# Kernel tuning notes

Hardware: AMD Instinct MI355X
Metric: run time of the kernel (lower is better)

Reference implementation:

```python
import jax, jax.numpy as jnp
import numpy as np

B, R, L, D, V, P = 128, 30, 60, 300, 50000, 3

def setup_inputs() -> dict:
    key = jax.random.key(0)
    ks = jax.random.split(key, 24)
    u = lambda k, shp: jax.random.uniform(k, shp, jnp.float32, -0.1, 0.1)
    inp = {
        'user_reviews': jax.random.randint(ks[0], (B, R, L), 0, V),
        'item_reviews': jax.random.randint(ks[1], (B, R, L), 0, V),
        'user_emb': u(ks[2], (V, D)),
        'item_emb': u(ks[3], (V, D)),
        'g1_w': u(ks[4], (D, D)), 'g1_b': u(ks[5], (D,)),
        'g2_w': u(ks[6], (D, D)), 'g2_b': u(ks[7], (D,)),
        # per-pointer review-level co-attention params (gumbel=True, pooling=max)
        'Mr': jax.random.normal(ks[8], (P, D, D)),
        'Wur': jax.random.normal(ks[9], (P, D, D)) * 0.05, 'bur': jnp.zeros((P, D)),
        'Wir': jax.random.normal(ks[10], (P, D, D)) * 0.05, 'bir': jnp.zeros((P, D)),
        # per-pointer word-level co-attention params (gumbel=False, pooling=avg)
        'Mw': jax.random.normal(ks[11], (P, D, D)),
        'Wuw': jax.random.normal(ks[12], (P, D, D)) * 0.05, 'buw': jnp.zeros((P, D)),
        'Wiw': jax.random.normal(ks[13], (P, D, D)) * 0.05, 'biw': jnp.zeros((P, D)),
        # FM params, pred_in_dim = 2*P*D (pointer_agg='concat')
        'fm_w0': jnp.zeros((1,)),
        'fm_w': jnp.zeros((2 * P * D,)),
        'fm_v': jax.random.normal(ks[14], (2 * P * D, 10)) * 0.01,
    }
    return inp

def _review_gate(embs, g1_w, g1_b, g2_w, g2_b):
    # embs: [B,R,L,D] -> [B,R,D]
    s = embs.sum(2)
    return jax.nn.sigmoid(s @ g1_w.T + g1_b) * jnp.tanh(s @ g2_w.T + g2_b)

def _coatt_scores(u_fea, i_fea, Wu, bu, Wi, bi, M):
    u = u_fea @ Wu.T + bu
    i = i_fea @ Wi.T + bi
    return jnp.einsum('brd,de,bse->brs', u, M, i)  # [B,R,R] or [B,L,L]

def reference(user_reviews, item_reviews, user_emb, item_emb,
              g1_w, g1_b, g2_w, g2_b,
              Mr, Wur, bur, Wir, bir,
              Mw, Wuw, buw, Wiw, biw,
              fm_w0, fm_w, fm_v):
    gkey = jax.random.key(42)
    u_embs = user_emb[user_reviews]  # [B,R,L,D]
    i_embs = item_emb[item_reviews]
    u_rev = _review_gate(u_embs, g1_w, g1_b, g2_w, g2_b)  # [B,R,D]
    i_rev = _review_gate(i_embs, g1_w, g1_b, g2_w, g2_b)
    u_reps, i_reps = [], []
    for p in range(P):
        # review-level co-attention, max pooling, gumbel hard (top-1 pointer)
        s = _coatt_scores(u_rev, i_rev, Wur[p], bur[p], Wir[p], bir[p], Mr[p])
        u_score = s.max(2)   # [B,R]
        i_score = s.max(1)   # [B,R]
        gu = jax.random.gumbel(jax.random.fold_in(gkey, 2 * p), u_score.shape)
        gi = jax.random.gumbel(jax.random.fold_in(gkey, 2 * p + 1), i_score.shape)
        # hard one-hot bmm gather + .long() re-embed == argmax review select
        # (the .long() cast in torch severs the straight-through grad path)
        idx_u = jnp.argmax(u_score + gu, axis=1)  # [B]
        idx_i = jnp.argmax(i_score + gi, axis=1)
        u_tok = jnp.take_along_axis(user_reviews, idx_u[:, None, None], axis=1)[:, 0]  # [B,L]
        i_tok = jnp.take_along_axis(item_reviews, idx_i[:, None, None], axis=1)[:, 0]
        u_words = user_emb[u_tok]  # [B,L,D]
        i_words = item_emb[i_tok]
        # word-level co-attention, avg pooling, soft attention
        s2 = _coatt_scores(u_words, i_words, Wuw[p], buw[p], Wiw[p], biw[p], Mw[p])
        p_u = jax.nn.softmax(s2.mean(2), axis=1)  # [B,L]
        p_i = jax.nn.softmax(s2.mean(1), axis=1)
        u_reps.append(jnp.einsum('bld,bl->bd', u_words, p_u))
        i_reps.append(jnp.einsum('bld,bl->bd', i_words, p_i))
    u_fea = jnp.concatenate(u_reps, axis=1)  # [B, P*D] (pointer_agg='concat')
    i_fea = jnp.concatenate(i_reps, axis=1)
    joint = jnp.concatenate([u_fea, i_fea], axis=1)  # [B, 2*P*D]; dropout is identity (eval)
    # Factorization Machine
    linear = fm_w0 + jnp.sum(fm_w * joint, axis=1, keepdims=True)
    inter = 0.5 * jnp.sum((joint @ fm_v) ** 2 - (joint ** 2) @ (fm_v ** 2), axis=1, keepdims=True)
    return (linear + inter)[:, 0]  # [B]
```

## Files before the change

### kernel.cpp

```cpp
#include <hip/hip_runtime.h>
#include <stdint.h>
#include <math.h>


__host__ __device__ static inline void tf2x32(uint32_t k0, uint32_t k1,
                                              uint32_t x0, uint32_t x1,
                                              uint32_t* o0, uint32_t* o1) {
  uint32_t ks[3] = {k0, k1, k0 ^ k1 ^ 0x1BD11BDAu};
  x0 += ks[0]; x1 += ks[1];
  const int rotA[4] = {13, 15, 26, 6};
  const int rotB[4] = {17, 29, 16, 24};
#pragma unroll
  for (int i = 0; i < 5; ++i) {
    const int* rot = ((i & 1) == 0) ? rotA : rotB;
#pragma unroll
    for (int j = 0; j < 4; ++j) {
      x0 += x1;
      x1 = (x1 << rot[j]) | (x1 >> (32 - rot[j]));
      x1 ^= x0;
    }
    x0 += ks[(i + 1) % 3];
    x1 += ks[(i + 2) % 3] + (uint32_t)(i + 1);
  }
  *o0 = x0; *o1 = x1;
}

struct GKeys { uint32_t v[12]; };
struct Ptr6 {
  const float* X[6];
  const float* W[6];
  const float* Bb[6];
  float*       Y[6];
};

__device__ static inline float jax_gumbel32(uint32_t k0, uint32_t k1, uint32_t idx) {
  uint32_t o0, o1;
  tf2x32(k0, k1, 0u, idx, &o0, &o1);
  uint32_t bits = o0 ^ o1;
  float f = __uint_as_float((bits >> 9) | 0x3f800000u) - 1.0f;
  float u = (f > 0.0f) ? f : 1.17549435e-38f;
  return -logf(-logf(u));
}

#define MODE_NN 0
#define MODE_NT 1
#define MODE_TN 2

template <int MODE, bool BIAS>
__device__ __forceinline__ void gemm_tile(float* __restrict__ sm,
                                          const float* __restrict__ X,
                                          const float* __restrict__ W,
                                          const float* __restrict__ bias,
                                          float* __restrict__ Y,
                                          float* __restrict__ Yt,
                                          int M, int bm, int n0, int t) {
  float (*Xs)[68] = (float(*)[68])sm;
  float (*Ws_)[68] = (float(*)[68])(sm + 20 * 68);
  const bool act = t < 256;
  int tm4 = ((t >> 4) & 15) * 4;
  int tn4 = (t & 15) * 4;
  float acc[4][4] = {{0.f}};
  int xm = t >> 2;
  int xk = (t & 3) * 5;
  for (int k0 = 0; k0 < 300; k0 += 20) {
    if (act) {
      if (MODE == MODE_TN) {
#pragma unroll
        for (int i = 0; i < 5; ++i) {
          int flat = t + i * 256;
          int kk = flat >> 6, nn = flat & 63;
          int r = bm + nn;
          Xs[kk][nn] = (r < 300) ? X[(size_t)(k0 + kk) * 300 + r] : 0.f;
        }
      } else {
        int rr = bm + xm; if (rr >= M) rr = M - 1;
        const float* xp = X + (size_t)rr * 300 + k0 + xk;
#pragma unroll
        for (int j = 0; j < 5; ++j) Xs[xk + j][xm] = xp[j];
      }
      if (MODE == MODE_NT) {
        int d = n0 + xm;
        bool ok = d < 300;
        const float* wp = W + (size_t)d * 300 + k0 + xk;
#pragma unroll
        for (int j = 0; j < 5; ++j) Ws_[xk + j][xm] = ok ? wp[j] : 0.f;
      } else {
#pragma unroll
        for (int i = 0; i < 5; ++i) {
          int flat = t + i * 256;
          int kk = flat >> 6, nn = flat & 63;
          int col = n0 + nn;
          Ws_[kk][nn] = (col < 300) ? W[(size_t)(k0 + kk) * 300 + col] : 0.f;
        }
      }
    }
    __syncthreads();
    if (act) {
#pragma unroll
      for (int kk = 0; kk < 20; ++kk) {
        const float4 a = *(const float4*)&Xs[kk][tm4];
        const float4 w = *(const float4*)&Ws_[kk][tn4];
        float av[4] = {a.x, a.y, a.z, a.w};
        float wv[4] = {w.x, w.y, w.z, w.w};
#pragma unroll
        for (int i = 0; i < 4; ++i)
#pragma unroll
          for (int j = 0; j < 4; ++j)
            acc[i][j] = fmaf(av[i], wv[j], acc[i][j]);
      }
    }
    __syncthreads();
  }
  if (!act) return;
  float bv[4] = {0.f, 0.f, 0.f, 0.f};
  if (BIAS) {
#pragma unroll
    for (int j = 0; j < 4; ++j) {
      int col = n0 + tn4 + j;
      if (col < 300) bv[j] = bias[col];
    }
  }
#pragma unroll
  for (int i = 0; i < 4; ++i) {
    int row = bm + tm4 + i;
    if (row < M) {
      float* yp = Y + (size_t)row * 300 + n0 + tn4;
#pragma unroll
      for (int j = 0; j < 4; ++j) {
        int col = n0 + tn4 + j;
        if (col < 300) yp[j] = acc[i][j] + bv[j];
      }
    }
  }
  if (Yt) {
#pragma unroll
    for (int i = 0; i < 4; ++i) {
      int row = bm + tm4 + i;
      if (row < 300) {
#pragma unroll
        for (int j = 0; j < 4; ++j) {
          int col = n0 + tn4 + j;
          if (col < 300) Yt[(size_t)col * 300 + row] = acc[i][j];
        }
      }
    }
  }
}

__global__ __launch_bounds__(256)
void weights_kernel(const float* __restrict__ Wur, const float* __restrict__ Mr,
                    const float* __restrict__ Mw, const float* __restrict__ Wiw,
                    const float* __restrict__ Wuw,
                    const float* __restrict__ bur, const float* __restrict__ buw,
                    const float* __restrict__ biw,
                    float* __restrict__ Wp, float* __restrict__ A1,
                    float* __restrict__ CGH, float* __restrict__ Bp) {
  __shared__ __align__(16) float arena[2720];
  int bid = blockIdx.x, t = threadIdx.x;
  if (bid < 75) {
    int z = bid / 25, r = bid % 25;
    gemm_tile<MODE_TN, false>(arena, Wur + (size_t)z * 90000, Mr + (size_t)z * 90000,
                              nullptr, Wp + (size_t)z * 90000, nullptr,
                              300, (r / 5) * 64, (r % 5) * 64, t);
  } else if (bid < 150) {
    int zi = bid - 75, z = zi / 25, r = zi % 25;
    gemm_tile<MODE_NN, false>(arena, Mw + (size_t)z * 90000, Wiw + (size_t)z * 90000,
                              nullptr, A1 + (size_t)z * 90000, nullptr,
                              300, (r / 5) * 64, (r % 5) * 64, t);
  } else {
    int z = bid - 150;
    float* vb = arena;
    float* t1s = arena + 304;
    float* t2s = arena + 608;
    const float* Mwz = Mw + (size_t)z * 90000;
    const float* Wuwz = Wuw + (size_t)z * 90000;
    const float* Wiwz = Wiw + (size_t)z * 90000;
    const float* Mrz = Mr + (size_t)z * 90000;
    for (int k = t; k < 300; k += 256) vb[k] = biw[z * 300 + k];
    __syncthreads();
    for (int e = t; e < 300; e += 256) {
      float a = 0.f;
      for (int k = 0; k < 300; ++k) a = fmaf(Mwz[(size_t)e * 300 + k], vb[k], a);
      t1s[e] = a;
    }
    __syncthreads();
    for (int k = t; k < 300; k += 256) {
      float a = 0.f;
      for (int d = 0; d < 300; ++d) a = fmaf(Wuwz[(size_t)d * 300 + k], t1s[d], a);
      CGH[(size_t)(2 * z) * 300 + k] = a;
    }
    __syncthreads();
    for (int d = t; d < 300; d += 256) vb[d] = buw[z * 300 + d];
    __syncthreads();
    for (int e = t; e < 300; e += 256) {
      float a = 0.f;
      for (int d = 0; d < 300; ++d) a = fmaf(Mwz[(size_t)d * 300 + e], vb[d], a);
      t2s[e] = a;
    }
    __syncthreads();
    for (int k = t; k < 300; k += 256) {
      float a = 0.f;
      for (int e = 0; e < 300; ++e) a = fmaf(Wiwz[(size_t)e * 300 + k], t2s[e], a);
      CGH[(size_t)(2 * z + 1) * 300 + k] = a;
    }
    __syncthreads();
    for (int d = t; d < 300; d += 256) vb[d] = bur[z * 300 + d];
    __syncthreads();
    for (int e = t; e < 300; e += 256) {
      float a = 0.f;
      for (int d = 0; d < 300; ++d) a = fmaf(Mrz[(size_t)d * 300 + e], vb[d], a);
      Bp[z * 300 + e] = a;
    }
  }
}

__global__ __launch_bounds__(320)
void gather_kernel(const int* __restrict__ uRevs, const int* __restrict__ iRevs,
                   const float* __restrict__ uEmb, const float* __restrict__ iEmb,
                   float* __restrict__ S) {
  int bid = blockIdx.x;
  int t = threadIdx.x;
  __shared__ int toks[4][60];
  if (t < 240) {
    int rr = t / 60, l = t - rr * 60;
    int grow = bid * 4 + rr;
    int side = grow / 3840;
    int row = grow - side * 3840;
    const int* revs = side ? iRevs : uRevs;
    toks[rr][l] = revs[row * 60 + l];
  }
  __syncthreads();
  if (t < 300) {
    int sub = t / 75;
    int q4 = (t - sub * 75) * 4;
    int grow = bid * 4 + sub;
    int side = grow / 3840;
    const float* emb = side ? iEmb : uEmb;
    const int* tk = toks[sub];
    float ax = 0.f, ay = 0.f, az = 0.f, aw = 0.f;
#pragma unroll
    for (int l0 = 0; l0 < 60; l0 += 10) {
      float4 v[10];
#pragma unroll
      for (int qq = 0; qq < 10; ++qq)
        v[qq] = *(const float4*)&emb[(size_t)tk[l0 + qq] * 300 + q4];
#pragma unroll
      for (int qq = 0; qq < 10; ++qq) {
        ax += v[qq].x; ay += v[qq].y; az += v[qq].z; aw += v[qq].w;
      }
    }
    float4 r = {ax, ay, az, aw};
    *(float4*)&S[(size_t)grow * 300 + q4] = r;
  }
}

__global__ __launch_bounds__(256)
void gate_kernel(const float* __restrict__ S,
                 const float* __restrict__ g1w, const float* __restrict__ g1b,
                 const float* __restrict__ g2w, const float* __restrict__ g2b,
                 float* __restrict__ REV,
                 const float* __restrict__ Wuw, const float* __restrict__ A1,
                 float* __restrict__ KG, float* __restrict__ KGT) {
  __shared__ __align__(16) float arena[4080];
  int bid = blockIdx.x, t = threadIdx.x;
  if (bid < 600) {
    float (*Xs)[68] = (float(*)[68])arena;
    float (*Ws1)[68] = (float(*)[68])(arena + 1360);
    float (*Ws2)[68] = (float(*)[68])(arena + 2720);
    int bm = (bid / 5) * 64;
    int n0 = (bid % 5) * 64;
    int tm4 = (t >> 4) * 4;
    int tn4 = (t & 15) * 4;
    float acc1[4][4] = {{0.f}};
    float acc2[4][4] = {{0.f}};
    int xm = t >> 2;
    int xk = (t & 3) * 5;
    for (int k0 = 0; k0 < 300; k0 += 20) {
      const float* xp = S + (size_t)(bm + xm) * 300 + k0 + xk;
#pragma unroll
      for (int j = 0; j < 5; ++j) Xs[xk + j][xm] = xp[j];
      {
        int dIdx = n0 + xm;
        bool ok = dIdx < 300;
        const float* wp1 = g1w + (size_t)dIdx * 300 + k0 + xk;
        const float* wp2 = g2w + (size_t)dIdx * 300 + k0 + xk;
#pragma unroll
        for (int j = 0; j < 5; ++j) Ws1[xk + j][xm] = ok ? wp1[j] : 0.f;
#pragma unroll
        for (int j = 0; j < 5; ++j) Ws2[xk + j][xm] = ok ? wp2[j] : 0.f;
      }
      __syncthreads();
#pragma unroll
      for (int kk = 0; kk < 20; ++kk) {
        const float4 a = *(const float4*)&Xs[kk][tm4];
        const float4 w1 = *(const float4*)&Ws1[kk][tn4];
        const float4 w2 = *(const float4*)&Ws2[kk][tn4];
        float av[4] = {a.x, a.y, a.z, a.w};
        float w1v[4] = {w1.x, w1.y, w1.z, w1.w};
        float w2v[4] = {w2.x, w2.y, w2.z, w2.w};
#pragma unroll
        for (int i = 0; i < 4; ++i)
#pragma unroll
          for (int j = 0; j < 4; ++j) {
            acc1[i][j] = fmaf(av[i], w1v[j], acc1[i][j]);
            acc2[i][j] = fmaf(av[i], w2v[j], acc2[i][j]);
          }
      }
      __syncthreads();
    }
#pragma unroll
    for (int i = 0; i < 4; ++i) {
      int row = bm + tm4 + i;
      float* yp = REV + (size_t)row * 300 + n0 + tn4;
#pragma unroll
      for (int j = 0; j < 4; ++j) {
        int col = n0 + tn4 + j;
        if (col < 300) {
          float a = acc1[i][j] + g1b[col];
          float b = acc2[i][j] + g2b[col];
          yp[j] = (1.f / (1.f + expf(-a))) * tanhf(b);
        }
      }
    }
  } else {
    int zi = bid - 600, z = zi / 25, r = zi % 25;
    gemm_tile<MODE_TN, false>(arena, Wuw + (size_t)z * 90000, A1 + (size_t)z * 90000,
                              nullptr, KG + (size_t)z * 90000,
                              KGT + (size_t)z * 90000,
                              300, (r / 5) * 64, (r % 5) * 64, t);
  }
}

__global__ __launch_bounds__(256)
void rev128_kernel(Ptr6 P) {
  int z = blockIdx.z;
  const bool nt = z >= 3;
  const float* __restrict__ X = P.X[z];
  const float* __restrict__ W = P.W[z];
  const float* __restrict__ bias = P.Bb[z];
  float* __restrict__ Y = P.Y[z];
  __shared__ __align__(16) float Xs[20][136];
  __shared__ __align__(16) float Ws_[20][68];
  int t = threadIdx.x;
  int bm = blockIdx.x * 128, n0 = blockIdx.y * 64;
  int tm8 = (t >> 4) * 8, tn4 = (t & 15) * 4;
  float acc[8][4] = {{0.f}};
  int xm = t >> 1, xk = (t & 1) * 10;
  int wm = t >> 2, wk = (t & 3) * 5;
  for (int k0 = 0; k0 < 300; k0 += 20) {
    const float* xp = X + (size_t)(bm + xm) * 300 + k0 + xk;
#pragma unroll
    for (int j = 0; j < 10; ++j) Xs[xk + j][xm] = xp[j];
    if (nt) {
      int d = n0 + wm;
      bool ok = d < 300;
      const float* wp = W + (size_t)d * 300 + k0 + wk;
#pragma unroll
      for (int j = 0; j < 5; ++j) Ws_[wk + j][wm] = ok ? wp[j] : 0.f;
    } else {
#pragma unroll
      for (int i = 0; i < 5; ++i) {
        int flat = t + i * 256;
        int kk = flat >> 6, nn = flat & 63;
        int col = n0 + nn;
        Ws_[kk][nn] = (col < 300) ? W[(size_t)(k0 + kk) * 300 + col] : 0.f;
      }
    }
    __syncthreads();
#pragma unroll
    for (int kk = 0; kk < 20; ++kk) {
      const float4 a0 = *(const float4*)&Xs[kk][tm8];
      const float4 a1 = *(const float4*)&Xs[kk][tm8 + 4];
      const float4 w = *(const float4*)&Ws_[kk][tn4];
      float av[8] = {a0.x, a0.y, a0.z, a0.w, a1.x, a1.y, a1.z, a1.w};
      float wv[4] = {w.x, w.y, w.z, w.w};
#pragma unroll
      for (int i = 0; i < 8; ++i)
#pragma unroll
        for (int j = 0; j < 4; ++j)
          acc[i][j] = fmaf(av[i], wv[j], acc[i][j]);
    }
    __syncthreads();
  }
  float bv[4];
#pragma unroll
  for (int j = 0; j < 4; ++j) {
    int col = n0 + tn4 + j;
    bv[j] = (col < 300) ? bias[col] : 0.f;
  }
#pragma unroll
  for (int i = 0; i < 8; ++i) {
    float* yp = Y + (size_t)(bm + tm8 + i) * 300 + n0 + tn4;
#pragma unroll
    for (int j = 0; j < 4; ++j) {
      int col = n0 + tn4 + j;
      if (col < 300) yp[j] = acc[i][j] + bv[j];
    }
  }
}

template <bool BIAS>
__global__ __launch_bounds__(256)
void nn6_kernel(Ptr6 P, int M) {
  __shared__ __align__(16) float arena[2720];
  int z = blockIdx.z;
  gemm_tile<MODE_NN, BIAS>(arena, P.X[z], P.W[z], P.Bb[z], P.Y[z], nullptr,
                           M, blockIdx.x * 64, blockIdx.y * 64, threadIdx.x);
}

__global__ __launch_bounds__(256)
void argmax_mean_kernel(const float* __restrict__ Tall, const float* __restrict__ Iall,
                        const int* __restrict__ uRevs, const int* __restrict__ iRevs,
                        const float* __restrict__ uEmb, const float* __restrict__ iEmb,
                        int* __restrict__ idxU, int* __restrict__ idxI,
                        float* __restrict__ MEAN, GKeys K) {
  int b = blockIdx.x, z = blockIdx.y, t = threadIdx.x;
  uint32_t ku0 = K.v[z * 4], ku1 = K.v[z * 4 + 1];
  uint32_t ki0 = K.v[z * 4 + 2], ki1 = K.v[z * 4 + 3];
  __shared__ float Is[30 * 301];
  __shared__ float Sc[900];
  __shared__ float us[30], vs[30];
  __shared__ int selU, selI;
  __shared__ int toksI_s[60], toksU_s[60];
  const float* Tb = Tall + (size_t)z * 1152000 + (size_t)b * 9000;
  const float* Ib = Iall + (size_t)z * 1152000 + (size_t)b * 9000;
  for (int e = t; e < 9000; e += 256) Is[(e / 300) * 301 + (e % 300)] = Ib[e];
  __syncthreads();
  for (int id = t; id < 900; id += 256) {
    int r = id / 30, c = id - r * 30;
    const float* tr = Tb + r * 300;
    const float* ic = Is + c * 301;
    float acc = 0.f;
    for (int k = 0; k < 300; ++k) acc = fmaf(tr[k], ic[k], acc);
    Sc[id] = acc;
  }
  __syncthreads();
  if (t < 30) {
    float m = -3.4e38f;
    for (int c = 0; c < 30; ++c) m = fmaxf(m, Sc[t * 30 + c]);
    us[t] = m + jax_gumbel32(ku0, ku1, (uint32_t)(b * 30 + t));
  } else if (t >= 64 && t < 94) {
    int s = t - 64;
    float m = -3.4e38f;
    for (int r = 0; r < 30; ++r) m = fmaxf(m, Sc[r * 30 + s]);
    vs[s] = m + jax_gumbel32(ki0, ki1, (uint32_t)(b * 30 + s));
  }
  __syncthreads();
  if (t == 0) {
    int best = 0; float bvv = us[0];
    for (int r = 1; r < 30; ++r) { if (us[r] > bvv) { bvv = us[r]; best = r; } }
    idxU[z * 128 + b] = best; selU = best;
  } else if (t == 1) {
    int best = 0; float bvv = vs[0];
    for (int s = 1; s < 30; ++s) { if (vs[s] > bvv) { bvv = vs[s]; best = s; } }
    idxI[z * 128 + b] = best; selI = best;
  }
  __syncthreads();
  if (t < 60) toksI_s[t] = iRevs[(b * 30 + selI) * 60 + t];
  else if (t >= 64 && t < 124) toksU_s[t - 64] = uRevs[(b * 30 + selU) * 60 + (t - 64)];
  __syncthreads();
  for (int dd = t; dd < 600; dd += 256) {
    int side = dd / 300;
    int d = dd - side * 300;
    const int* tk = side ? toksU_s : toksI_s;
    const float* em = side ? uEmb : iEmb;
    float acc = 0.f;
#pragma unroll
    for (int l0 = 0; l0 < 60; l0 += 10) {
      float v[10];
#pragma unroll
      for (int q = 0; q < 10; ++q)
        v[q] = em[(size_t)tk[l0 + q] * 300 + d];
#pragma unroll
      for (int q = 0; q < 10; ++q) acc += v[q];
    }
    MEAN[((size_t)(2 * z + side) * 128 + b) * 300 + d] = acc * (1.f / 60.f);
  }
}

__global__ __launch_bounds__(256)
void word_rep_kernel(const int* __restrict__ uRevs, const int* __restrict__ iRevs,
                     const float* __restrict__ uEmb, const float* __restrict__ iEmb,
                     const int* __restrict__ idxU, const int* __restrict__ idxI,
                     const float* __restrict__ GH, float* __restrict__ JNT) {
  int b = blockIdx.x, side = blockIdx.y, p = blockIdx.z;
  const int* revs = side ? iRevs : uRevs;
  const float* emb = side ? iEmb : uEmb;
  int idx = side ? idxI[p * 128 + b] : idxU[p * 128 + b];
  const float* gv = GH + ((size_t)(p * 2 + side) * 128 + b) * 300;
  __shared__ int toks[60];
  __shared__ float g_s[300];
  __shared__ float score[60];
  __shared__ float probs[64];
  int t = threadIdx.x;
  if (t < 60) toks[t] = revs[(b * 30 + idx) * 60 + t];
  for (int d = t; d < 300; d += 256) g_s[d] = gv[d];
  __syncthreads();
  int w = t >> 6, j = t & 63;
  for (int i = 0; i < 15; ++i) {
    int l = w * 15 + i;
    const float* er = emb + (size_t)toks[l] * 300;
    float partial = 0.f;
#pragma unroll
    for (int c = 0; c < 5; ++c) {
      int k = j + c * 64;
      if (k < 300) partial = fmaf(er[k], g_s[k], partial);
    }
#pragma unroll
    for (int m = 32; m >= 1; m >>= 1) partial += __shfl_xor(partial, m);
    if (j == 0) score[l] = partial;
  }
  __syncthreads();
  if (w == 0) {
    float s = (j < 60) ? score[j] : -3.4e38f;
    float m = s;
#pragma unroll
    for (int mm = 32; mm >= 1; mm >>= 1) m = fmaxf(m, __shfl_xor(m, mm));
    float e = (j < 60) ? expf(s - m) : 0.f;
    float sum = e;
#pragma unroll
    for (int mm = 32; mm >= 1; mm >>= 1) sum += __shfl_xor(sum, mm);
    if (j < 60) probs[j] = e / sum;
  }
  __syncthreads();
  float* outp = JNT + (size_t)b * 1800 + side * 900 + p * 300;
  for (int d = t; d < 300; d += 256) {
    float acc = 0.f;
    for (int l0 = 0; l0 < 60; l0 += 6) {
      float e0 = emb[(size_t)toks[l0 + 0] * 300 + d];
      float e1 = emb[(size_t)toks[l0 + 1] * 300 + d];
      float e2 = emb[(size_t)toks[l0 + 2] * 300 + d];
      float e3 = emb[(size_t)toks[l0 + 3] * 300 + d];
      float e4 = emb[(size_t)toks[l0 + 4] * 300 + d];
      float e5 = emb[(size_t)toks[l0 + 5] * 300 + d];
      acc = fmaf(probs[l0 + 0], e0, acc);
      acc = fmaf(probs[l0 + 1], e1, acc);
      acc = fmaf(probs[l0 + 2], e2, acc);
      acc = fmaf(probs[l0 + 3], e3, acc);
      acc = fmaf(probs[l0 + 4], e4, acc);
      acc = fmaf(probs[l0 + 5], e5, acc);
    }
    outp[d] = acc;
  }
}

__global__ __launch_bounds__(64)
void fm_kernel(const float* __restrict__ JNT, const float* __restrict__ w0,
               const float* __restrict__ fw, const float* __restrict__ fv,
               float* __restrict__ out) {
  int b = blockIdx.x, lane = threadIdx.x;
  const float* x = JNT + (size_t)b * 1800;
  float lin = 0.f;
  float t1[10], t2[10];
#pragma unroll
  for (int k = 0; k < 10; ++k) { t1[k] = 0.f; t2[k] = 0.f; }
  for (int j = lane; j < 1800; j += 64) {
    float xv = x[j];
    lin = fmaf(fw[j], xv, lin);
    float xx = xv * xv;
#pragma unroll
    for (int k = 0; k < 10; ++k) {
      float v = fv[j * 10 + k];
      t1[k] = fmaf(xv, v, t1[k]);
      t2[k] = fmaf(xx, v * v, t2[k]);
    }
  }
#pragma unroll
  for (int m = 32; m >= 1; m >>= 1) {
    lin += __shfl_xor(lin, m);
#pragma unroll
    for (int k = 0; k < 10; ++k) {
      t1[k] += __shfl_xor(t1[k], m);
      t2[k] += __shfl_xor(t2[k], m);
    }
  }
  if (lane == 0) {
    float inter = 0.f;
#pragma unroll
    for (int k = 0; k < 10; ++k) inter += t1[k] * t1[k] - t2[k];
    out[b] = w0[0] + lin + 0.5f * inter;
  }
}

extern "C" void kernel_launch(void* const* d_in, const int* in_sizes, int n_in,
                              void* d_out, int out_size, void* d_ws, size_t ws_size,
                              hipStream_t stream) {
  (void)in_sizes; (void)n_in; (void)out_size;
  const int*   uRevs = (const int*)d_in[0];
  const int*   iRevs = (const int*)d_in[1];
  const float* uEmb  = (const float*)d_in[2];
  const float* iEmb  = (const float*)d_in[3];
  const float* g1w   = (const float*)d_in[4];
  const float* g1b   = (const float*)d_in[5];
  const float* g2w   = (const float*)d_in[6];
  const float* g2b   = (const float*)d_in[7];
  const float* Mr    = (const float*)d_in[8];
  const float* Wur   = (const float*)d_in[9];
  const float* bur   = (const float*)d_in[10];
  const float* Wir   = (const float*)d_in[11];
  const float* bir   = (const float*)d_in[12];
  const float* Mw    = (const float*)d_in[13];
  const float* Wuw   = (const float*)d_in[14];
  const float* buw   = (const float*)d_in[15];
  const float* Wiw   = (const float*)d_in[16];
  const float* biw   = (const float*)d_in[17];
  const float* fmw0  = (const float*)d_in[18];
  const float* fmw   = (const float*)d_in[19];
  const float* fmv   = (const float*)d_in[20];
  float* out = (float*)d_out;

  float* ws = (float*)d_ws;
  const size_t NEED_BYTES = (size_t)10298700 * 4;
  if (ws_size < NEED_BYTES) return;

  float* S     = ws + 0;
  float* TPall = ws + 0;
  float* REV   = ws + 3456000;
  float* MEAN  = ws + 3456000;
  float* GH    = ws + 3686400;
  float* JNT   = ws + 3916800;
  int*   idxU  = (int*)(ws + 4147200);
  int*   idxI  = idxU + 384;
  float* IPall = ws + 5760000;
  float* A1    = ws + 9216000;
  float* Wp    = ws + 9486000;
  float* KG    = ws + 9756000;
  float* KGT   = ws + 10026000;
  float* Bp    = ws + 10296000;
  float* CGH   = ws + 10296900;

  weights_kernel<<<dim3(153), dim3(256), 0, stream>>>(
      Wur, Mr, Mw, Wiw, Wuw, bur, buw, biw, Wp, A1, CGH, Bp);

  gather_kernel<<<dim3(1920), dim3(320), 0, stream>>>(
      uRevs, iRevs, uEmb, iEmb, S);

  gate_kernel<<<dim3(675), dim3(256), 0, stream>>>(
      S, g1w, g1b, g2w, g2b, REV, Wuw, A1, KG, KGT);

  {
    Ptr6 P;
    for (int z = 0; z < 3; ++z) {
      P.X[z] = REV;
      P.W[z] = Wp + (size_t)z * 90000;
      P.Bb[z] = Bp + z * 300;
      P.Y[z] = TPall + (size_t)z * 1152000;
      P.X[z + 3] = REV + (size_t)3840 * 300;
      P.W[z + 3] = Wir + (size_t)z * 90000;
      P.Bb[z + 3] = bir + z * 300;
      P.Y[z + 3] = IPall + (size_t)z * 1152000;
    }
    rev128_kernel<<<dim3(30, 5, 6), dim3(256), 0, stream>>>(P);
  }

  {
    GKeys K;
    for (int p = 0; p < 3; ++p) {
      tf2x32(0u, 42u, 0u, (uint32_t)(2 * p),     &K.v[p * 4],     &K.v[p * 4 + 1]);
      tf2x32(0u, 42u, 0u, (uint32_t)(2 * p + 1), &K.v[p * 4 + 2], &K.v[p * 4 + 3]);
    }
    argmax_mean_kernel<<<dim3(128, 3), dim3(256), 0, stream>>>(
        TPall, IPall, uRevs, iRevs, uEmb, iEmb, idxU, idxI, MEAN, K);
  }

  {
    Ptr6 P;
    for (int zz = 0; zz < 6; ++zz) {
      int p = zz >> 1;
      P.X[zz] = MEAN + (size_t)zz * 38400;
      P.W[zz] = (zz & 1) ? KG + (size_t)p * 90000 : KGT + (size_t)p * 90000;
      P.Bb[zz] = CGH + (size_t)zz * 300;
      P.Y[zz] = GH + (size_t)zz * 38400;
    }
    nn6_kernel<true><<<dim3(2, 5, 6), dim3(256), 0, stream>>>(P, 128);
  }

  word_rep_kernel<<<dim3(128, 2, 3), dim3(256), 0, stream>>>(
      uRevs, iRevs, uEmb, iEmb, idxU, idxI, GH, JNT);

  fm_kernel<<<dim3(128), dim3(64), 0, stream>>>(JNT, fmw0, fmw, fmv, out);
}
```

Measured before the change: 397.1 us.

## Fuse gate projection into word_rep, enlarge gate tiles, vectorize argmax scoring

The separate nn6 launch for the word-level gate projection is removed. Each word_rep block now computes its own 300-element GEMV from MEAN and the KG/KGT matrices in shared memory, which saves a launch and the GH round trip at the cost of redundant matrix reads per block. The gate GEMM tiles grow from 64 to 128 rows with 8x4 per-thread outputs, and argmax_mean switches to float4 loads with 304-float padded rows. The gather loop batch also goes from 10 to 15 in-flight loads.

Result: slower. 414.2 us (+4.3%).

```diff
diff --git a/kernel.cpp b/kernel.cpp
--- a/kernel.cpp
+++ b/kernel.cpp
@@ -239,13 +239,13 @@
     const int* tk = toks[sub];
     float ax = 0.f, ay = 0.f, az = 0.f, aw = 0.f;
 #pragma unroll
-    for (int l0 = 0; l0 < 60; l0 += 10) {
-      float4 v[10];
-#pragma unroll
-      for (int qq = 0; qq < 10; ++qq)
+    for (int l0 = 0; l0 < 60; l0 += 15) {
+      float4 v[15];
+#pragma unroll
+      for (int qq = 0; qq < 15; ++qq)
         v[qq] = *(const float4*)&emb[(size_t)tk[l0 + qq] * 300 + q4];
 #pragma unroll
-      for (int qq = 0; qq < 10; ++qq) {
+      for (int qq = 0; qq < 15; ++qq) {
         ax += v[qq].x; ay += v[qq].y; az += v[qq].z; aw += v[qq].w;
       }
     }
@@ -261,45 +261,45 @@
                  float* __restrict__ REV,
                  const float* __restrict__ Wuw, const float* __restrict__ A1,
                  float* __restrict__ KG, float* __restrict__ KGT) {
-  __shared__ __align__(16) float arena[4080];
+  __shared__ __align__(16) float arena[5440];
   int bid = blockIdx.x, t = threadIdx.x;
-  if (bid < 600) {
-    float (*Xs)[68] = (float(*)[68])arena;
-    float (*Ws1)[68] = (float(*)[68])(arena + 1360);
-    float (*Ws2)[68] = (float(*)[68])(arena + 2720);
-    int bm = (bid / 5) * 64;
+  if (bid < 300) {
+    float (*Xs)[136] = (float(*)[136])arena;
+    float (*Ws1)[68] = (float(*)[68])(arena + 2720);
+    float (*Ws2)[68] = (float(*)[68])(arena + 4080);
+    int bm = (bid / 5) * 128;
     int n0 = (bid % 5) * 64;
-    int tm4 = (t >> 4) * 4;
-    int tn4 = (t & 15) * 4;
-    float acc1[4][4] = {{0.f}};
-    float acc2[4][4] = {{0.f}};
-    int xm = t >> 2;
-    int xk = (t & 3) * 5;
+    int tm8 = (t >> 4) * 8, tn4 = (t & 15) * 4;
+    float acc1[8][4] = {{0.f}};
+    float acc2[8][4] = {{0.f}};
+    int xm = t >> 1, xk = (t & 1) * 10;
+    int wm = t >> 2, wk = (t & 3) * 5;
     for (int k0 = 0; k0 < 300; k0 += 20) {
       const float* xp = S + (size_t)(bm + xm) * 300 + k0 + xk;
 #pragma unroll
-      for (int j = 0; j < 5; ++j) Xs[xk + j][xm] = xp[j];
+      for (int j = 0; j < 10; ++j) Xs[xk + j][xm] = xp[j];
       {
-        int dIdx = n0 + xm;
-        bool ok = dIdx < 300;
-        const float* wp1 = g1w + (size_t)dIdx * 300 + k0 + xk;
-        const float* wp2 = g2w + (size_t)dIdx * 300 + k0 + xk;
-#pragma unroll
-        for (int j = 0; j < 5; ++j) Ws1[xk + j][xm] = ok ? wp1[j] : 0.f;
-#pragma unroll
-        for (int j = 0; j < 5; ++j) Ws2[xk + j][xm] = ok ? wp2[j] : 0.f;
+        int d = n0 + wm;
+        bool ok = d < 300;
+        const float* wp1 = g1w + (size_t)d * 300 + k0 + wk;
+        const float* wp2 = g2w + (size_t)d * 300 + k0 + wk;
+#pragma unroll
+        for (int j = 0; j < 5; ++j) Ws1[wk + j][wm] = ok ? wp1[j] : 0.f;
+#pragma unroll
+        for (int j = 0; j < 5; ++j) Ws2[wk + j][wm] = ok ? wp2[j] : 0.f;
       }
       __syncthreads();
 #pragma unroll
       for (int kk = 0; kk < 20; ++kk) {
-        const float4 a = *(const float4*)&Xs[kk][tm4];
+        const float4 a0 = *(const float4*)&Xs[kk][tm8];
+        const float4 a1 = *(const float4*)&Xs[kk][tm8 + 4];
         const float4 w1 = *(const float4*)&Ws1[kk][tn4];
         const float4 w2 = *(const float4*)&Ws2[kk][tn4];
-        float av[4] = {a.x, a.y, a.z, a.w};
+        float av[8] = {a0.x, a0.y, a0.z, a0.w, a1.x, a1.y, a1.z, a1.w};
         float w1v[4] = {w1.x, w1.y, w1.z, w1.w};
         float w2v[4] = {w2.x, w2.y, w2.z, w2.w};
 #pragma unroll
-        for (int i = 0; i < 4; ++i)
+        for (int i = 0; i < 8; ++i)
 #pragma unroll
           for (int j = 0; j < 4; ++j) {
             acc1[i][j] = fmaf(av[i], w1v[j], acc1[i][j]);
@@ -309,8 +309,8 @@
       __syncthreads();
     }
 #pragma unroll
-    for (int i = 0; i < 4; ++i) {
-      int row = bm + tm4 + i;
+    for (int i = 0; i < 8; ++i) {
+      int row = bm + tm8 + i;
       float* yp = REV + (size_t)row * 300 + n0 + tn4;
 #pragma unroll
       for (int j = 0; j < 4; ++j) {
@@ -323,7 +323,7 @@
       }
     }
   } else {
-    int zi = bid - 600, z = zi / 25, r = zi % 25;
+    int zi = bid - 300, z = zi / 25, r = zi % 25;
     gemm_tile<MODE_TN, false>(arena, Wuw + (size_t)z * 90000, A1 + (size_t)z * 90000,
                               nullptr, KG + (size_t)z * 90000,
                               KGT + (size_t)z * 90000,
@@ -399,15 +399,6 @@
   }
 }
 
-template <bool BIAS>
-__global__ __launch_bounds__(256)
-void nn6_kernel(Ptr6 P, int M) {
-  __shared__ __align__(16) float arena[2720];
-  int z = blockIdx.z;
-  gemm_tile<MODE_NN, BIAS>(arena, P.X[z], P.W[z], P.Bb[z], P.Y[z], nullptr,
-                           M, blockIdx.x * 64, blockIdx.y * 64, threadIdx.x);
-}
-
 __global__ __launch_bounds__(256)
 void argmax_mean_kernel(const float* __restrict__ Tall, const float* __restrict__ Iall,
                         const int* __restrict__ uRevs, const int* __restrict__ iRevs,
@@ -417,21 +408,31 @@
   int b = blockIdx.x, z = blockIdx.y, t = threadIdx.x;
   uint32_t ku0 = K.v[z * 4], ku1 = K.v[z * 4 + 1];
   uint32_t ki0 = K.v[z * 4 + 2], ki1 = K.v[z * 4 + 3];
-  __shared__ float Is[30 * 301];
+  __shared__ __align__(16) float Is[30 * 304];
   __shared__ float Sc[900];
   __shared__ float us[30], vs[30];
   __shared__ int selU, selI;
   __shared__ int toksI_s[60], toksU_s[60];
   const float* Tb = Tall + (size_t)z * 1152000 + (size_t)b * 9000;
   const float* Ib = Iall + (size_t)z * 1152000 + (size_t)b * 9000;
-  for (int e = t; e < 9000; e += 256) Is[(e / 300) * 301 + (e % 300)] = Ib[e];
+  for (int fc = t; fc < 2250; fc += 256) {
+    int r = fc / 75, q = fc - r * 75;
+    *(float4*)&Is[r * 304 + q * 4] = *(const float4*)&Ib[r * 300 + q * 4];
+  }
   __syncthreads();
   for (int id = t; id < 900; id += 256) {
     int r = id / 30, c = id - r * 30;
     const float* tr = Tb + r * 300;
-    const float* ic = Is + c * 301;
+    const float* ic = Is + c * 304;
     float acc = 0.f;
-    for (int k = 0; k < 300; ++k) acc = fmaf(tr[k], ic[k], acc);
+    for (int k = 0; k < 300; k += 4) {
+      float4 a = *(const float4*)&tr[k];
+      float4 w = *(const float4*)&ic[k];
+      acc = fmaf(a.x, w.x, acc);
+      acc = fmaf(a.y, w.y, acc);
+      acc = fmaf(a.z, w.z, acc);
+      acc = fmaf(a.w, w.w, acc);
+    }
     Sc[id] = acc;
   }
   __syncthreads();
@@ -482,19 +483,37 @@
 void word_rep_kernel(const int* __restrict__ uRevs, const int* __restrict__ iRevs,
                      const float* __restrict__ uEmb, const float* __restrict__ iEmb,
                      const int* __restrict__ idxU, const int* __restrict__ idxI,
-                     const float* __restrict__ GH, float* __restrict__ JNT) {
+                     const float* __restrict__ MEAN, const float* __restrict__ KG,
+                     const float* __restrict__ KGT, const float* __restrict__ CGH,
+                     float* __restrict__ JNT) {
   int b = blockIdx.x, side = blockIdx.y, p = blockIdx.z;
+  int zz = 2 * p + side;
   const int* revs = side ? iRevs : uRevs;
   const float* emb = side ? iEmb : uEmb;
   int idx = side ? idxI[p * 128 + b] : idxU[p * 128 + b];
-  const float* gv = GH + ((size_t)(p * 2 + side) * 128 + b) * 300;
+  const float* Kmat = (side ? KGT : KG) + (size_t)p * 90000;
   __shared__ int toks[60];
+  __shared__ float ms[300];
   __shared__ float g_s[300];
   __shared__ float score[60];
   __shared__ float probs[64];
   int t = threadIdx.x;
   if (t < 60) toks[t] = revs[(b * 30 + idx) * 60 + t];
-  for (int d = t; d < 300; d += 256) g_s[d] = gv[d];
+  const float* mrow = MEAN + ((size_t)zz * 128 + b) * 300;
+  for (int d = t; d < 300; d += 256) ms[d] = mrow[d];
+  __syncthreads();
+  for (int k = t; k < 300; k += 256) {
+    const float* kr = Kmat + (size_t)k * 300;
+    float acc = 0.f;
+    for (int e = 0; e < 300; e += 4) {
+      float4 kv = *(const float4*)&kr[e];
+      acc = fmaf(kv.x, ms[e], acc);
+      acc = fmaf(kv.y, ms[e + 1], acc);
+      acc = fmaf(kv.z, ms[e + 2], acc);
+      acc = fmaf(kv.w, ms[e + 3], acc);
+    }
+    g_s[k] = acc + CGH[(size_t)zz * 300 + k];
+  }
   __syncthreads();
   int w = t >> 6, j = t & 63;
   for (int i = 0; i < 15; ++i) {
@@ -617,7 +636,6 @@
   float* TPall = ws + 0;
   float* REV   = ws + 3456000;
   float* MEAN  = ws + 3456000;
-  float* GH    = ws + 3686400;
   float* JNT   = ws + 3916800;
   int*   idxU  = (int*)(ws + 4147200);
   int*   idxI  = idxU + 384;
@@ -635,7 +653,7 @@
   gather_kernel<<<dim3(1920), dim3(320), 0, stream>>>(
       uRevs, iRevs, uEmb, iEmb, S);
 
-  gate_kernel<<<dim3(675), dim3(256), 0, stream>>>(
+  gate_kernel<<<dim3(375), dim3(256), 0, stream>>>(
       S, g1w, g1b, g2w, g2b, REV, Wuw, A1, KG, KGT);
 
   {
@@ -663,20 +681,8 @@
         TPall, IPall, uRevs, iRevs, uEmb, iEmb, idxU, idxI, MEAN, K);
   }
 
-  {
-    Ptr6 P;
-    for (int zz = 0; zz < 6; ++zz) {
-      int p = zz >> 1;
-      P.X[zz] = MEAN + (size_t)zz * 38400;
-      P.W[zz] = (zz & 1) ? KG + (size_t)p * 90000 : KGT + (size_t)p * 90000;
-      P.Bb[zz] = CGH + (size_t)zz * 300;
-      P.Y[zz] = GH + (size_t)zz * 38400;
-    }
-    nn6_kernel<true><<<dim3(2, 5, 6), dim3(256), 0, stream>>>(P, 128);
-  }
-
   word_rep_kernel<<<dim3(128, 2, 3), dim3(256), 0, stream>>>(
-      uRevs, iRevs, uEmb, iEmb, idxU, idxI, GH, JNT);
+      uRevs, iRevs, uEmb, iEmb, idxU, idxI, MEAN, KG, KGT, CGH, JNT);
 
   fm_kernel<<<dim3(128), dim3(64), 0, stream>>>(JNT, fmw0, fmw, fmv, out);
 }
```
